# Kernel tuning notes

Hardware: AMD Instinct MI355X
Metric: run time of the kernel (lower is better)

Reference implementation:

```python
import jax, jax.numpy as jnp
import numpy as np
import math

B, C, HW = 4, 256, 32          # batch, seq_len (=channels), spatial side
D_MODEL = HW * HW              # 1024
OUT_C = 32 * 32                # 1024
D_STATE = 16
EXPAND = 2
D_INNER = EXPAND * D_MODEL     # 2048
DT_RANK = math.ceil(D_MODEL / 16)  # 64
D_CONV = 4


def setup_inputs() -> dict:
    key = jax.random.key(0)
    ks = jax.random.split(key, 12)
    s = 0.02
    x1 = jax.random.normal(ks[0], (B, C, HW, HW), dtype=jnp.float32)
    in_proj_w = jax.random.normal(ks[1], (2 * D_INNER, D_MODEL), dtype=jnp.float32) * s
    conv_w = jax.random.normal(ks[2], (D_INNER, 1, D_CONV), dtype=jnp.float32) * s
    conv_b = jnp.zeros((D_INNER,), dtype=jnp.float32)
    x_proj_w = jax.random.normal(ks[3], (DT_RANK + 2 * D_STATE, D_INNER), dtype=jnp.float32) * s
    dt_proj_w = jax.random.normal(ks[4], (D_INNER, DT_RANK), dtype=jnp.float32) * s
    dt_proj_b = jnp.zeros((D_INNER,), dtype=jnp.float32)
    A_log = jnp.log(jnp.broadcast_to(jnp.arange(1, D_STATE + 1, dtype=jnp.float32), (D_INNER, D_STATE)))
    D = jnp.ones((D_INNER,), dtype=jnp.float32)
    out_proj_w = jax.random.normal(ks[5], (OUT_C, D_INNER), dtype=jnp.float32) * s
    ln_w = jnp.ones((OUT_C,), dtype=jnp.float32)
    ln_b = jnp.zeros((OUT_C,), dtype=jnp.float32)
    return {"x1": x1, "in_proj_w": in_proj_w, "conv_w": conv_w, "conv_b": conv_b,
            "x_proj_w": x_proj_w, "dt_proj_w": dt_proj_w, "dt_proj_b": dt_proj_b,
            "A_log": A_log, "D": D, "out_proj_w": out_proj_w, "ln_w": ln_w, "ln_b": ln_b}


def _mamba_forward(x, in_proj_w, conv_w, conv_b, x_proj_w, dt_proj_w, dt_proj_b, A_log, D, out_proj_w):
    # x: (B, L, d_model)
    xz = jnp.einsum('bld,ed->ble', x, in_proj_w)            # (B,L,2*d_inner)
    xs, res = jnp.split(xz, 2, axis=-1)                     # each (B,L,d_inner)
    # depthwise causal conv1d, padding=d_conv-1 then truncate to L (== left pad)
    xs_c = jnp.transpose(xs, (0, 2, 1))                     # (B,d_inner,L)
    xs_c = jax.lax.conv_general_dilated(
        xs_c, conv_w, window_strides=(1,), padding=[(D_CONV - 1, 0)],
        dimension_numbers=('NCH', 'OIH', 'NCH'), feature_group_count=D_INNER)
    xs_c = xs_c + conv_b[None, :, None]
    xs = jax.nn.silu(jnp.transpose(xs_c, (0, 2, 1)))        # (B,L,d_inner)
    # input-dependent SSM parameters
    x_dbl = jnp.einsum('bld,ed->ble', xs, x_proj_w)         # (B,L,dt_rank+2N)
    dt, Bm, Cm = jnp.split(x_dbl, [DT_RANK, DT_RANK + D_STATE], axis=-1)
    delta = jax.nn.softplus(jnp.einsum('blr,dr->bld', dt, dt_proj_w) + dt_proj_b)  # (B,L,d_inner)
    A = -jnp.exp(A_log)                                     # (d_inner, N)
    deltaA = jnp.exp(delta[..., None] * A)                  # (B,L,d_inner,N)
    deltaB_u = delta[..., None] * Bm[:, :, None, :] * xs[..., None]  # (B,L,d_inner,N)

    def step(h, inp):
        dA, dBu, Ct = inp                                   # (B,d,N),(B,d,N),(B,N)
        h = dA * h + dBu
        y = jnp.einsum('bdn,bn->bd', h, Ct)
        return h, y

    h0 = jnp.zeros((deltaA.shape[0], D_INNER, D_STATE), dtype=deltaA.dtype)
    _, ys = jax.lax.scan(step, h0, (jnp.transpose(deltaA, (1, 0, 2, 3)),
                                    jnp.transpose(deltaB_u, (1, 0, 2, 3)),
                                    jnp.transpose(Cm, (1, 0, 2))))
    y = jnp.transpose(ys, (1, 0, 2))                        # (B,L,d_inner)
    y = y + D * xs
    y = y * jax.nn.silu(res)
    return jnp.einsum('bld,od->blo', y, out_proj_w)         # (B,L,out_c)


def reference(x1, in_proj_w, conv_w, conv_b, x_proj_w, dt_proj_w, dt_proj_b,
              A_log, D, out_proj_w, ln_w, ln_b):
    b, c, h, w = x1.shape
    x = x1.reshape(b, c, h * w)                             # (B, L=c, d_model)
    y = _mamba_forward(x, in_proj_w, conv_w, conv_b, x_proj_w, dt_proj_w,
                       dt_proj_b, A_log, D, out_proj_w)
    mu = jnp.mean(y, axis=-1, keepdims=True)
    var = jnp.var(y, axis=-1, keepdims=True)
    y = (y - mu) * jax.lax.rsqrt(var + 1e-5) * ln_w + ln_b
    return y.reshape(b, c, 32, 32)
```

## Files before the change

kernel.cpp:

```cpp
#include <hip/hip_runtime.h>
#include <hip/hip_bf16.h>
#include <math.h>

#define BATCH 4
#define SEQL 256
#define DMODEL 1024
#define DINNER 2048
#define DSTATE 16
#define DTRANK 64
#define OUTC 1024
#define NROWS (BATCH * SEQL)
#define NCHUNK 4
#define CH 64

typedef __attribute__((ext_vector_type(8))) short bf16x8;
typedef __attribute__((ext_vector_type(4))) float f32x4;

__global__ __launch_bounds__(256) void gemm_mfma(const __hip_bfloat16* __restrict__ A,
                                                 const __hip_bfloat16* __restrict__ B,
                                                 float* __restrict__ C,
                                                 int M, int N, int K,
                                                 int lda, int ldb) {
    __shared__ __hip_bfloat16 As[2][128 * 32];
    __shared__ __hip_bfloat16 Bs[2][128 * 32];
    const int t  = threadIdx.x;
    const int w  = t >> 6;
    const int ln = t & 63;
    const int wm = w >> 1, wn = w & 1;
    const int q  = ln >> 4, lr = ln & 15;
    const int m0 = blockIdx.y * 128;
    const int n0 = blockIdx.x * 128;
    const int Kpart = K / gridDim.z;
    const int kbase = blockIdx.z * Kpart;

    f32x4 acc[4][4] = {};

    const __hip_bfloat16* Ag = A + (size_t)m0 * lda + kbase;
    const __hip_bfloat16* Bg = B + (size_t)n0 * ldb + kbase;

    auto stage = [&](int k0, int buf) {
        #pragma unroll
        for (int i = 0; i < 2; ++i) {
            const int c = (i * 4 + w) * 64 + ln;
            const int r = c >> 2, col = (c & 3) * 8;
            __builtin_amdgcn_global_load_lds(
                (const __attribute__((address_space(1))) void*)(Ag + (size_t)r * lda + k0 + col),
                (__attribute__((address_space(3))) void*)(As[buf] + (i * 4 + w) * 64 * 8),
                16, 0, 0);
            __builtin_amdgcn_global_load_lds(
                (const __attribute__((address_space(1))) void*)(Bg + (size_t)r * ldb + k0 + col),
                (__attribute__((address_space(3))) void*)(Bs[buf] + (i * 4 + w) * 64 * 8),
                16, 0, 0);
        }
    };

    const int nk = Kpart / 32;
    stage(0, 0);
    __syncthreads();
    for (int kk = 0; kk < nk; ++kk) {
        if (kk + 1 < nk) stage((kk + 1) * 32, (kk + 1) & 1);
        const int buf = kk & 1;
        bf16x8 af[4], bfr[4];
        #pragma unroll
        for (int i = 0; i < 4; ++i)
            af[i] = *(const bf16x8*)(As[buf] + (wm * 64 + i * 16 + lr) * 32 + q * 8);
        #pragma unroll
        for (int j = 0; j < 4; ++j)
            bfr[j] = *(const bf16x8*)(Bs[buf] + (wn * 64 + j * 16 + lr) * 32 + q * 8);
        #pragma unroll
        for (int i = 0; i < 4; ++i)
            #pragma unroll
            for (int j = 0; j < 4; ++j)
                acc[i][j] = __builtin_amdgcn_mfma_f32_16x16x32_bf16(af[i], bfr[j], acc[i][j], 0, 0, 0);
        __syncthreads();
    }
    float* Cz = C + (size_t)blockIdx.z * M * N;
    #pragma unroll
    for (int i = 0; i < 4; ++i) {
        const int mrow = m0 + wm * 64 + i * 16 + q * 4;
        #pragma unroll
        for (int j = 0; j < 4; ++j) {
            const int ncol = n0 + wn * 64 + j * 16 + lr;
            #pragma unroll
            for (int r = 0; r < 4; ++r)
                Cz[(size_t)(mrow + r) * N + ncol] = acc[i][j][r];
        }
    }
}

__global__ __launch_bounds__(256) void gemm_dtsp(const __hip_bfloat16* __restrict__ A,
                                                 const __hip_bfloat16* __restrict__ B,
                                                 const float* __restrict__ bd,
                                                 float* __restrict__ delta) {
    __shared__ __hip_bfloat16 As[128 * 32];
    __shared__ __hip_bfloat16 Bs[128 * 32];
    const int t  = threadIdx.x;
    const int w  = t >> 6;
    const int ln = t & 63;
    const int wm = w >> 1, wn = w & 1;
    const int q  = ln >> 4, lr = ln & 15;
    const int m0 = blockIdx.y * 128;
    const int n0 = blockIdx.x * 128;
    const int lda = 128, ldb = 64, N = 2048;

    f32x4 acc[4][4] = {};
    const __hip_bfloat16* Ag = A + (size_t)m0 * lda;
    const __hip_bfloat16* Bg = B + (size_t)n0 * ldb;

    for (int k0 = 0; k0 < 64; k0 += 32) {
        #pragma unroll
        for (int i = 0; i < 2; ++i) {
            const int c = (i * 4 + w) * 64 + ln;
            const int r = c >> 2, col = (c & 3) * 8;
            __builtin_amdgcn_global_load_lds(
                (const __attribute__((address_space(1))) void*)(Ag + (size_t)r * lda + k0 + col),
                (__attribute__((address_space(3))) void*)(As + (i * 4 + w) * 64 * 8),
                16, 0, 0);
            __builtin_amdgcn_global_load_lds(
                (const __attribute__((address_space(1))) void*)(Bg + (size_t)r * ldb + k0 + col),
                (__attribute__((address_space(3))) void*)(Bs + (i * 4 + w) * 64 * 8),
                16, 0, 0);
        }
        __syncthreads();
        bf16x8 af[4], bfr[4];
        #pragma unroll
        for (int i = 0; i < 4; ++i)
            af[i] = *(const bf16x8*)(As + (wm * 64 + i * 16 + lr) * 32 + q * 8);
        #pragma unroll
        for (int j = 0; j < 4; ++j)
            bfr[j] = *(const bf16x8*)(Bs + (wn * 64 + j * 16 + lr) * 32 + q * 8);
        #pragma unroll
        for (int i = 0; i < 4; ++i)
            #pragma unroll
            for (int j = 0; j < 4; ++j)
                acc[i][j] = __builtin_amdgcn_mfma_f32_16x16x32_bf16(af[i], bfr[j], acc[i][j], 0, 0, 0);
        __syncthreads();
    }
    #pragma unroll
    for (int i = 0; i < 4; ++i) {
        const int mrow = m0 + wm * 64 + i * 16 + q * 4;
        #pragma unroll
        for (int j = 0; j < 4; ++j) {
            const int ncol = n0 + wn * 64 + j * 16 + lr;
            const float bias = bd[ncol];
            #pragma unroll
            for (int r = 0; r < 4; ++r) {
                float v = acc[i][j][r] + bias;
                float sp = (v > 20.f) ? v : log1pf(__expf(v));
                delta[(size_t)(mrow + r) * N + ncol] = sp;
            }
        }
    }
}

__global__ void xdbl_reduce_kernel(const float* __restrict__ part,
                                   float* __restrict__ xdbl,
                                   __hip_bfloat16* __restrict__ xdblb) {
    const int i = blockIdx.x * 256 + threadIdx.x;
    float s = 0.f;
    #pragma unroll
    for (int z = 0; z < 8; ++z) s += part[(size_t)z * (1024 * 128) + i];
    xdbl[i] = s;
    xdblb[i] = __float2bfloat16(s);
}

#define R0 (1024 * 1024)
#define R1 (R0 + 4096 * 1024)
#define R2 (R1 + 2048 * 1024)
#define R3 (R2 + 128 * 2048)
#define R4 (R3 + 2048 * 64)
__global__ void cast_all_kernel(const float* __restrict__ x1,
                                const float* __restrict__ w_in,
                                const float* __restrict__ w_out,
                                const float* __restrict__ w_xp,
                                const float* __restrict__ w_dt,
                                __hip_bfloat16* __restrict__ xa,
                                __hip_bfloat16* __restrict__ wb1,
                                __hip_bfloat16* __restrict__ wob,
                                __hip_bfloat16* __restrict__ wpb,
                                __hip_bfloat16* __restrict__ wdb) {
    int i = blockIdx.x * 256 + threadIdx.x;
    if (i < R0) {
        xa[i] = __float2bfloat16(x1[i]);
    } else if (i < R1) {
        int j = i - R0; wb1[j] = __float2bfloat16(w_in[j]);
    } else if (i < R2) {
        int j = i - R1; wob[j] = __float2bfloat16(w_out[j]);
    } else if (i < R3) {
        int j = i - R2; int e = j >> 11;
        wpb[j] = __float2bfloat16(e < 96 ? w_xp[j] : 0.f);
    } else if (i < R4) {
        int j = i - R3; wdb[j] = __float2bfloat16(w_dt[j]);
    }
}

__global__ void conv_silu_kernel(const float* __restrict__ xz,
                                 const float* __restrict__ conv_w,
                                 const float* __restrict__ conv_b,
                                 float* __restrict__ xs,
                                 __hip_bfloat16* __restrict__ xsb) {
    int idx = blockIdx.x * blockDim.x + threadIdx.x;
    int d = idx & (DINNER - 1);
    int l = (idx >> 11) & (SEQL - 1);
    int b = idx >> 19;
    const float w0 = conv_w[d * 4 + 0];
    const float w1 = conv_w[d * 4 + 1];
    const float w2 = conv_w[d * 4 + 2];
    const float w3 = conv_w[d * 4 + 3];
    float acc = conv_b[d];
    const size_t base = (size_t)(b * SEQL) * (2 * DINNER) + d;
    if (l >= 3) acc += w0 * xz[base + (size_t)(l - 3) * (2 * DINNER)];
    if (l >= 2) acc += w1 * xz[base + (size_t)(l - 2) * (2 * DINNER)];
    if (l >= 1) acc += w2 * xz[base + (size_t)(l - 1) * (2 * DINNER)];
    acc += w3 * xz[base + (size_t)l * (2 * DINNER)];
    float v = acc / (1.f + __expf(-acc));
    xs[idx] = v;
    xsb[idx] = __float2bfloat16(v);
}

__device__ __forceinline__ float row_reduce16(float x) {
    x += __int_as_float(__builtin_amdgcn_update_dpp(0, __float_as_int(x), 0x128, 0xF, 0xF, true));
    x += __int_as_float(__builtin_amdgcn_update_dpp(0, __float_as_int(x), 0x124, 0xF, 0xF, true));
    x += __int_as_float(__builtin_amdgcn_update_dpp(0, __float_as_int(x), 0x122, 0xF, 0xF, true));
    x += __int_as_float(__builtin_amdgcn_update_dpp(0, __float_as_int(x), 0x121, 0xF, 0xF, true));
    return x;
}

__global__ __launch_bounds__(256) void scan_carry_kernel(const float* __restrict__ delta,
                                                         const float* __restrict__ xs,
                                                         const float* __restrict__ xdbl,
                                                         const float* __restrict__ A_log,
                                                         float* __restrict__ carryL,
                                                         float* __restrict__ carryP) {
    __shared__ float sDU[CH][16][2];
    __shared__ float sB[CH][16];
    const int b = blockIdx.y, c = blockIdx.z, dg = blockIdx.x;
    const int t = threadIdx.x;
    const int dl = t >> 4, n = t & 15;
    const int d = dg * 16 + dl;
    const float a = -__expf(A_log[d * DSTATE + n]);
    const int srow = t >> 4, scol = t & 15;
    const int sd = dg * 16 + scol;
    const int rowbase = b * SEQL + c * CH;
    #pragma unroll
    for (int i = 0; i < 4; ++i) {
        const int row = rowbase + i * 16 + srow;
        const float dv = delta[(size_t)row * DINNER + sd];
        const float xv = xs[(size_t)row * DINNER + sd];
        sDU[i * 16 + srow][scol][0] = dv;
        sDU[i * 16 + srow][scol][1] = dv * xv;
        sB[i * 16 + srow][scol] = xdbl[row * 128 + 64 + scol];
    }
    __syncthreads();
    float h = 0.f, P = 1.f;
    #pragma unroll 16
    for (int l = 0; l < CH; ++l) {
        const float e = __expf(sDU[l][dl][0] * a);
        h = e * h + sDU[l][dl][1] * sB[l][n];
        P *= e;
    }
    const size_t ci = (((size_t)(b * NCHUNK + c)) * DINNER + d) * DSTATE + n;
    carryL[ci] = h;
    carryP[ci] = P;
}

__global__ __launch_bounds__(256) void scan_apply_kernel(const float* __restrict__ delta,
                                                         const float* __restrict__ xs,
                                                         const float* __restrict__ xdbl,
                                                         const float* __restrict__ xz,
                                                         const float* __restrict__ A_log,
                                                         const float* __restrict__ Dp,
                                                         const float* __restrict__ carryL,
                                                         const float* __restrict__ carryP,
                                                         __hip_bfloat16* __restrict__ ybb) {
    __shared__ float sDU[CH][16][2];
    __shared__ float sBC[CH][16][2];
    __shared__ float sGW[CH][16][2];
    const int b = blockIdx.y, c = blockIdx.z, dg = blockIdx.x;
    const int t = threadIdx.x;
    const int dl = t >> 4, n = t & 15;
    const int d = dg * 16 + dl;
    const float a = -__expf(A_log[d * DSTATE + n]);
    const int srow = t >> 4, scol = t & 15;
    const int sd = dg * 16 + scol;
    const float Dstage = Dp[sd];
    const int rowbase = b * SEQL + c * CH;
    #pragma unroll
    for (int i = 0; i < 4; ++i) {
        const int row = rowbase + i * 16 + srow;
        const float dv = delta[(size_t)row * DINNER + sd];
        const float xv = xs[(size_t)row * DINNER + sd];
        const float r  = xz[(size_t)row * (2 * DINNER) + DINNER + sd];
        const float g = r / (1.f + __expf(-r));
        const int lr_ = i * 16 + srow;
        sDU[lr_][scol][0] = dv;
        sDU[lr_][scol][1] = dv * xv;
        sGW[lr_][scol][0] = g;
        sGW[lr_][scol][1] = Dstage * xv * g;
        sBC[lr_][scol][0] = xdbl[row * 128 + 64 + scol];
        sBC[lr_][scol][1] = xdbl[row * 128 + 80 + scol];
    }
    __syncthreads();
    float h = 0.f;
    for (int j = 0; j < c; ++j) {
        const size_t ci = (((size_t)(b * NCHUNK + j)) * DINNER + d) * DSTATE + n;
        h = carryP[ci] * h + carryL[ci];
    }
    #pragma unroll 16
    for (int l = 0; l < CH; ++l) {
        const float e = __expf(sDU[l][dl][0] * a);
        h = e * h + sDU[l][dl][1] * sBC[l][n][0];
        float p = row_reduce16(h * sBC[l][n][1]);
        if (n == 0) {
            const float y = p * sGW[l][dl][0] + sGW[l][dl][1];
            ybb[(size_t)(rowbase + l) * DINNER + d] = __float2bfloat16(y);
        }
    }
}

__global__ __launch_bounds__(256) void ln_kernel(const float* __restrict__ opart,
                                                 const float* __restrict__ lw,
                                                 const float* __restrict__ lb,
                                                 float* __restrict__ out) {
    __shared__ float red[8];
    const int row = blockIdx.x;
    const int t = threadIdx.x;
    float v[4];
    float s = 0.f, s2 = 0.f;
    #pragma unroll
    for (int i = 0; i < 4; ++i) {
        const int c = t + 256 * i;
        float acc = 0.f;
        #pragma unroll
        for (int z = 0; z < 4; ++z)
            acc += opart[(size_t)z * (1024 * 1024) + (size_t)row * OUTC + c];
        v[i] = acc;
        s += acc;
        s2 += acc * acc;
    }
    #pragma unroll
    for (int o = 32; o; o >>= 1) {
        s += __shfl_down(s, o);
        s2 += __shfl_down(s2, o);
    }
    const int wid = t >> 6;
    if ((t & 63) == 0) { red[wid] = s; red[4 + wid] = s2; }
    __syncthreads();
    if (t == 0) {
        float ts = red[0] + red[1] + red[2] + red[3];
        float ts2 = red[4] + red[5] + red[6] + red[7];
        float mu = ts * (1.f / OUTC);
        float var = ts2 * (1.f / OUTC) - mu * mu;
        red[0] = mu;
        red[1] = rsqrtf(var + 1e-5f);
    }
    __syncthreads();
    const float mu = red[0], rs = red[1];
    #pragma unroll
    for (int i = 0; i < 4; ++i) {
        const int c = t + 256 * i;
        out[(size_t)row * OUTC + c] = (v[i] - mu) * rs * lw[c] + lb[c];
    }
}

extern "C" void kernel_launch(void* const* d_in, const int* in_sizes, int n_in,
                              void* d_out, int out_size, void* d_ws, size_t ws_size,
                              hipStream_t stream) {
    const float* x1        = (const float*)d_in[0];
    const float* in_proj_w = (const float*)d_in[1];
    const float* conv_w    = (const float*)d_in[2];
    const float* conv_b    = (const float*)d_in[3];
    const float* x_proj_w  = (const float*)d_in[4];
    const float* dt_proj_w = (const float*)d_in[5];
    const float* dt_proj_b = (const float*)d_in[6];
    const float* A_log     = (const float*)d_in[7];
    const float* Dp        = (const float*)d_in[8];
    const float* out_proj_w= (const float*)d_in[9];
    const float* ln_w      = (const float*)d_in[10];
    const float* ln_b      = (const float*)d_in[11];
    float* out = (float*)d_out;

    char* p = (char*)d_ws;
    __hip_bfloat16* xa    = (__hip_bfloat16*)p; p += (size_t)1024 * 1024 * 2;
    __hip_bfloat16* wb1   = (__hip_bfloat16*)p; p += (size_t)4096 * 1024 * 2;
    __hip_bfloat16* wpb   = (__hip_bfloat16*)p; p += (size_t)128 * 2048 * 2;
    __hip_bfloat16* wob   = (__hip_bfloat16*)p; p += (size_t)1024 * 2048 * 2;
    __hip_bfloat16* wdb   = (__hip_bfloat16*)p; p += (size_t)2048 * 64 * 2;
    __hip_bfloat16* xsb   = (__hip_bfloat16*)p; p += (size_t)1024 * 2048 * 2;
    __hip_bfloat16* ybb   = (__hip_bfloat16*)p; p += (size_t)1024 * 2048 * 2;
    __hip_bfloat16* xdblb = (__hip_bfloat16*)p; p += (size_t)1024 * 128 * 2;
    float* xz    = (float*)p; p += (size_t)1024 * 4096 * 4;
    float* xs    = (float*)p; p += (size_t)1024 * 2048 * 4;
    float* xdbl  = (float*)p; p += (size_t)1024 * 128 * 4;
    float* xpart = (float*)p; p += (size_t)8 * 1024 * 128 * 4;
    float* delta = (float*)p; p += (size_t)1024 * 2048 * 4;
    float* carryL = (float*)p; p += (size_t)BATCH * NCHUNK * DINNER * DSTATE * 4;
    float* carryP = (float*)p; p += (size_t)BATCH * NCHUNK * DINNER * DSTATE * 4;
    float* opart = xz;

    cast_all_kernel<<<(R4 + 255) / 256, 256, 0, stream>>>(x1, in_proj_w, out_proj_w,
                                                          x_proj_w, dt_proj_w,
                                                          xa, wb1, wob, wpb, wdb);
    gemm_mfma<<<dim3(32, 8, 1), 256, 0, stream>>>(xa, wb1, xz,
                                                  NROWS, 2 * DINNER, DMODEL, DMODEL, DMODEL);
    conv_silu_kernel<<<(NROWS * DINNER) / 256, 256, 0, stream>>>(xz, conv_w, conv_b, xs, xsb);
    gemm_mfma<<<dim3(1, 8, 8), 256, 0, stream>>>(xsb, wpb, xpart,
                                                 NROWS, 128, DINNER, DINNER, DINNER);
    xdbl_reduce_kernel<<<(1024 * 128) / 256, 256, 0, stream>>>(xpart, xdbl, xdblb);
    gemm_dtsp<<<dim3(16, 8), 256, 0, stream>>>(xdblb, wdb, dt_proj_b, delta);
    scan_carry_kernel<<<dim3(DINNER / 16, BATCH, NCHUNK), 256, 0, stream>>>(
        delta, xs, xdbl, A_log, carryL, carryP);
    scan_apply_kernel<<<dim3(DINNER / 16, BATCH, NCHUNK), 256, 0, stream>>>(
        delta, xs, xdbl, xz, A_log, Dp, carryL, carryP, ybb);
    gemm_mfma<<<dim3(8, 8, 4), 256, 0, stream>>>(ybb, wob, opart,
                                                 NROWS, OUTC, DINNER, DINNER, DINNER);
    ln_kernel<<<NROWS, 256, 0, stream>>>(opart, ln_w, ln_b, out);
}
```

Measured before the change: 221.1 us.

## Fuse fp32-to-bf16 casts into GEMMs and drop xdbl reduce kernel

```diff
diff --git a/kernel.cpp b/kernel.cpp
--- a/kernel.cpp
+++ b/kernel.cpp
@@ -16,13 +16,94 @@
 typedef __attribute__((ext_vector_type(8))) short bf16x8;
 typedef __attribute__((ext_vector_type(4))) float f32x4;
 
+__device__ __forceinline__ short f2b(float x) {
+    union { __hip_bfloat16 h; short s; } u;
+    u.h = __float2bfloat16(x);
+    return u.s;
+}
+__device__ __forceinline__ float b2f(short x) {
+    union { __hip_bfloat16 h; short s; } u;
+    u.s = x;
+    return __bfloat162float(u.h);
+}
+__device__ __forceinline__ bf16x8 cvt8(const float* p) {
+    bf16x8 r;
+    #pragma unroll
+    for (int j = 0; j < 8; ++j) r[j] = f2b(p[j]);
+    return r;
+}
+
+__global__ __launch_bounds__(256) void gemm_in(const float* __restrict__ A,
+                                               const float* __restrict__ B,
+                                               __hip_bfloat16* __restrict__ C) {
+    const int K = 1024, N = 4096;
+    __shared__ float As[2][128 * 32];
+    __shared__ float Bs[2][128 * 32];
+    const int t  = threadIdx.x;
+    const int w  = t >> 6;
+    const int ln = t & 63;
+    const int wm = w >> 1, wn = w & 1;
+    const int q  = ln >> 4, lr = ln & 15;
+    const int m0 = blockIdx.y * 128;
+    const int n0 = blockIdx.x * 128;
+
+    f32x4 acc[4][4] = {};
+    const float* Ag = A + (size_t)m0 * K;
+    const float* Bg = B + (size_t)n0 * K;
+
+    auto stage = [&](int k0, int buf) {
+        #pragma unroll
+        for (int i = 0; i < 4; ++i) {
+            const int c = (i * 4 + w) * 64 + ln;
+            const int r = c >> 3, col = (c & 7) * 4;
+            __builtin_amdgcn_global_load_lds(
+                (const __attribute__((address_space(1))) void*)(Ag + (size_t)r * K + k0 + col),
+                (__attribute__((address_space(3))) void*)(As[buf] + c * 4), 16, 0, 0);
+            __builtin_amdgcn_global_load_lds(
+                (const __attribute__((address_space(1))) void*)(Bg + (size_t)r * K + k0 + col),
+                (__attribute__((address_space(3))) void*)(Bs[buf] + c * 4), 16, 0, 0);
+        }
+    };
+
+    stage(0, 0);
+    __syncthreads();
+    for (int kk = 0; kk < 32; ++kk) {
+        if (kk + 1 < 32) stage((kk + 1) * 32, (kk + 1) & 1);
+        const int buf = kk & 1;
+        bf16x8 af[4], bfr[4];
+        #pragma unroll
+        for (int i = 0; i < 4; ++i)
+            af[i] = cvt8(As[buf] + (wm * 64 + i * 16 + lr) * 32 + q * 8);
+        #pragma unroll
+        for (int j = 0; j < 4; ++j)
+            bfr[j] = cvt8(Bs[buf] + (wn * 64 + j * 16 + lr) * 32 + q * 8);
+        #pragma unroll
+        for (int i = 0; i < 4; ++i)
+            #pragma unroll
+            for (int j = 0; j < 4; ++j)
+                acc[i][j] = __builtin_amdgcn_mfma_f32_16x16x32_bf16(af[i], bfr[j], acc[i][j], 0, 0, 0);
+        __syncthreads();
+    }
+    #pragma unroll
+    for (int i = 0; i < 4; ++i) {
+        const int mrow = m0 + wm * 64 + i * 16 + q * 4;
+        #pragma unroll
+        for (int j = 0; j < 4; ++j) {
+            const int ncol = n0 + wn * 64 + j * 16 + lr;
+            #pragma unroll
+            for (int r = 0; r < 4; ++r)
+                C[(size_t)(mrow + r) * N + ncol] = __float2bfloat16(acc[i][j][r]);
+        }
+    }
+}
+
 __global__ __launch_bounds__(256) void gemm_mfma(const __hip_bfloat16* __restrict__ A,
                                                  const __hip_bfloat16* __restrict__ B,
                                                  float* __restrict__ C,
                                                  int M, int N, int K,
                                                  int lda, int ldb) {
-    __shared__ __hip_bfloat16 As[2][128 * 32];
-    __shared__ __hip_bfloat16 Bs[2][128 * 32];
+    __shared__ __hip_bfloat16 As[128 * 32];
+    __shared__ __hip_bfloat16 Bs[128 * 32];
     const int t  = threadIdx.x;
     const int w  = t >> 6;
     const int ln = t & 63;
@@ -34,39 +115,29 @@
     const int kbase = blockIdx.z * Kpart;
 
     f32x4 acc[4][4] = {};
-
     const __hip_bfloat16* Ag = A + (size_t)m0 * lda + kbase;
     const __hip_bfloat16* Bg = B + (size_t)n0 * ldb + kbase;
 
-    auto stage = [&](int k0, int buf) {
+    for (int k0 = 0; k0 < Kpart; k0 += 32) {
         #pragma unroll
         for (int i = 0; i < 2; ++i) {
             const int c = (i * 4 + w) * 64 + ln;
             const int r = c >> 2, col = (c & 3) * 8;
             __builtin_amdgcn_global_load_lds(
                 (const __attribute__((address_space(1))) void*)(Ag + (size_t)r * lda + k0 + col),
-                (__attribute__((address_space(3))) void*)(As[buf] + (i * 4 + w) * 64 * 8),
-                16, 0, 0);
+                (__attribute__((address_space(3))) void*)(As + c * 8), 16, 0, 0);
             __builtin_amdgcn_global_load_lds(
                 (const __attribute__((address_space(1))) void*)(Bg + (size_t)r * ldb + k0 + col),
-                (__attribute__((address_space(3))) void*)(Bs[buf] + (i * 4 + w) * 64 * 8),
-                16, 0, 0);
-        }
-    };
-
-    const int nk = Kpart / 32;
-    stage(0, 0);
-    __syncthreads();
-    for (int kk = 0; kk < nk; ++kk) {
-        if (kk + 1 < nk) stage((kk + 1) * 32, (kk + 1) & 1);
-        const int buf = kk & 1;
+                (__attribute__((address_space(3))) void*)(Bs + c * 8), 16, 0, 0);
+        }
+        __syncthreads();
         bf16x8 af[4], bfr[4];
         #pragma unroll
         for (int i = 0; i < 4; ++i)
-            af[i] = *(const bf16x8*)(As[buf] + (wm * 64 + i * 16 + lr) * 32 + q * 8);
+            af[i] = *(const bf16x8*)(As + (wm * 64 + i * 16 + lr) * 32 + q * 8);
         #pragma unroll
         for (int j = 0; j < 4; ++j)
-            bfr[j] = *(const bf16x8*)(Bs[buf] + (wn * 64 + j * 16 + lr) * 32 + q * 8);
+            bfr[j] = *(const bf16x8*)(Bs + (wn * 64 + j * 16 + lr) * 32 + q * 8);
         #pragma unroll
         for (int i = 0; i < 4; ++i)
             #pragma unroll
@@ -88,11 +159,77 @@
     }
 }
 
-__global__ __launch_bounds__(256) void gemm_dtsp(const __hip_bfloat16* __restrict__ A,
-                                                 const __hip_bfloat16* __restrict__ B,
+__global__ __launch_bounds__(256) void gemm_out(const __hip_bfloat16* __restrict__ A,
+                                                const float* __restrict__ B,
+                                                float* __restrict__ C) {
+    const int M = 1024, N = 1024, K = 2048;
+    __shared__ __hip_bfloat16 As[128 * 32];
+    __shared__ float Bs[128 * 32];
+    const int t  = threadIdx.x;
+    const int w  = t >> 6;
+    const int ln = t & 63;
+    const int wm = w >> 1, wn = w & 1;
+    const int q  = ln >> 4, lr = ln & 15;
+    const int m0 = blockIdx.y * 128;
+    const int n0 = blockIdx.x * 128;
+    const int Kpart = K / 4;
+    const int kbase = blockIdx.z * Kpart;
+
+    f32x4 acc[4][4] = {};
+    const __hip_bfloat16* Ag = A + (size_t)m0 * K + kbase;
+    const float* Bg = B + (size_t)n0 * K + kbase;
+
+    for (int k0 = 0; k0 < Kpart; k0 += 32) {
+        #pragma unroll
+        for (int i = 0; i < 2; ++i) {
+            const int c = (i * 4 + w) * 64 + ln;
+            const int r = c >> 2, col = (c & 3) * 8;
+            __builtin_amdgcn_global_load_lds(
+                (const __attribute__((address_space(1))) void*)(Ag + (size_t)r * K + k0 + col),
+                (__attribute__((address_space(3))) void*)(As + c * 8), 16, 0, 0);
+        }
+        #pragma unroll
+        for (int i = 0; i < 4; ++i) {
+            const int c = (i * 4 + w) * 64 + ln;
+            const int r = c >> 3, col = (c & 7) * 4;
+            __builtin_amdgcn_global_load_lds(
+                (const __attribute__((address_space(1))) void*)(Bg + (size_t)r * K + k0 + col),
+                (__attribute__((address_space(3))) void*)(Bs + c * 4), 16, 0, 0);
+        }
+        __syncthreads();
+        bf16x8 af[4], bfr[4];
+        #pragma unroll
+        for (int i = 0; i < 4; ++i)
+            af[i] = *(const bf16x8*)(As + (wm * 64 + i * 16 + lr) * 32 + q * 8);
+        #pragma unroll
+        for (int j = 0; j < 4; ++j)
+            bfr[j] = cvt8(Bs + (wn * 64 + j * 16 + lr) * 32 + q * 8);
+        #pragma unroll
+        for (int i = 0; i < 4; ++i)
+            #pragma unroll
+            for (int j = 0; j < 4; ++j)
+                acc[i][j] = __builtin_amdgcn_mfma_f32_16x16x32_bf16(af[i], bfr[j], acc[i][j], 0, 0, 0);
+        __syncthreads();
+    }
+    float* Cz = C + (size_t)blockIdx.z * M * N;
+    #pragma unroll
+    for (int i = 0; i < 4; ++i) {
+        const int mrow = m0 + wm * 64 + i * 16 + q * 4;
+        #pragma unroll
+        for (int j = 0; j < 4; ++j) {
+            const int ncol = n0 + wn * 64 + j * 16 + lr;
+            #pragma unroll
+            for (int r = 0; r < 4; ++r)
+                Cz[(size_t)(mrow + r) * N + ncol] = acc[i][j][r];
+        }
+    }
+}
+
+__global__ __launch_bounds__(256) void gemm_dtsp(const float* __restrict__ xpart,
+                                                 const __hip_bfloat16* __restrict__ Bw,
                                                  const float* __restrict__ bd,
                                                  float* __restrict__ delta) {
-    __shared__ __hip_bfloat16 As[128 * 32];
+    __shared__ __hip_bfloat16 As[128 * 64];
     __shared__ __hip_bfloat16 Bs[128 * 32];
     const int t  = threadIdx.x;
     const int w  = t >> 6;
@@ -101,31 +238,35 @@
     const int q  = ln >> 4, lr = ln & 15;
     const int m0 = blockIdx.y * 128;
     const int n0 = blockIdx.x * 128;
-    const int lda = 128, ldb = 64, N = 2048;
+    const int N = 2048;
+
+    #pragma unroll
+    for (int j = 0; j < 32; ++j) {
+        const int e = j * 256 + t;
+        const int row = e >> 6, col = e & 63;
+        float s = 0.f;
+        #pragma unroll
+        for (int z = 0; z < 8; ++z)
+            s += xpart[(size_t)z * (1024 * 128) + (size_t)(m0 + row) * 128 + col];
+        As[row * 64 + col] = __float2bfloat16(s);
+    }
 
     f32x4 acc[4][4] = {};
-    const __hip_bfloat16* Ag = A + (size_t)m0 * lda;
-    const __hip_bfloat16* Bg = B + (size_t)n0 * ldb;
-
+    const __hip_bfloat16* Bg = Bw + (size_t)n0 * 64;
     for (int k0 = 0; k0 < 64; k0 += 32) {
         #pragma unroll
         for (int i = 0; i < 2; ++i) {
             const int c = (i * 4 + w) * 64 + ln;
             const int r = c >> 2, col = (c & 3) * 8;
             __builtin_amdgcn_global_load_lds(
-                (const __attribute__((address_space(1))) void*)(Ag + (size_t)r * lda + k0 + col),
-                (__attribute__((address_space(3))) void*)(As + (i * 4 + w) * 64 * 8),
-                16, 0, 0);
-            __builtin_amdgcn_global_load_lds(
-                (const __attribute__((address_space(1))) void*)(Bg + (size_t)r * ldb + k0 + col),
-                (__attribute__((address_space(3))) void*)(Bs + (i * 4 + w) * 64 * 8),
-                16, 0, 0);
+                (const __attribute__((address_space(1))) void*)(Bg + (size_t)r * 64 + k0 + col),
+                (__attribute__((address_space(3))) void*)(Bs + c * 8), 16, 0, 0);
         }
         __syncthreads();
         bf16x8 af[4], bfr[4];
         #pragma unroll
         for (int i = 0; i < 4; ++i)
-            af[i] = *(const bf16x8*)(As + (wm * 64 + i * 16 + lr) * 32 + q * 8);
+            af[i] = *(const bf16x8*)(As + (wm * 64 + i * 16 + lr) * 64 + k0 + q * 8);
         #pragma unroll
         for (int j = 0; j < 4; ++j)
             bfr[j] = *(const bf16x8*)(Bs + (wn * 64 + j * 16 + lr) * 32 + q * 8);
@@ -146,76 +287,48 @@
             #pragma unroll
             for (int r = 0; r < 4; ++r) {
                 float v = acc[i][j][r] + bias;
-                float sp = (v > 20.f) ? v : log1pf(__expf(v));
-                delta[(size_t)(mrow + r) * N + ncol] = sp;
+                delta[(size_t)(mrow + r) * N + ncol] = (v > 20.f) ? v : log1pf(__expf(v));
             }
         }
     }
 }
 
-__global__ void xdbl_reduce_kernel(const float* __restrict__ part,
-                                   float* __restrict__ xdbl,
-                                   __hip_bfloat16* __restrict__ xdblb) {
-    const int i = blockIdx.x * 256 + threadIdx.x;
-    float s = 0.f;
-    #pragma unroll
-    for (int z = 0; z < 8; ++z) s += part[(size_t)z * (1024 * 128) + i];
-    xdbl[i] = s;
-    xdblb[i] = __float2bfloat16(s);
-}
-
-#define R0 (1024 * 1024)
-#define R1 (R0 + 4096 * 1024)
-#define R2 (R1 + 2048 * 1024)
-#define R3 (R2 + 128 * 2048)
-#define R4 (R3 + 2048 * 64)
-__global__ void cast_all_kernel(const float* __restrict__ x1,
-                                const float* __restrict__ w_in,
-                                const float* __restrict__ w_out,
-                                const float* __restrict__ w_xp,
-                                const float* __restrict__ w_dt,
-                                __hip_bfloat16* __restrict__ xa,
-                                __hip_bfloat16* __restrict__ wb1,
-                                __hip_bfloat16* __restrict__ wob,
-                                __hip_bfloat16* __restrict__ wpb,
-                                __hip_bfloat16* __restrict__ wdb) {
-    int i = blockIdx.x * 256 + threadIdx.x;
-    if (i < R0) {
-        xa[i] = __float2bfloat16(x1[i]);
-    } else if (i < R1) {
-        int j = i - R0; wb1[j] = __float2bfloat16(w_in[j]);
-    } else if (i < R2) {
-        int j = i - R1; wob[j] = __float2bfloat16(w_out[j]);
-    } else if (i < R3) {
-        int j = i - R2; int e = j >> 11;
-        wpb[j] = __float2bfloat16(e < 96 ? w_xp[j] : 0.f);
-    } else if (i < R4) {
-        int j = i - R3; wdb[j] = __float2bfloat16(w_dt[j]);
-    }
-}
-
-__global__ void conv_silu_kernel(const float* __restrict__ xz,
+__global__ void conv_silu_kernel(const __hip_bfloat16* __restrict__ xz,
                                  const float* __restrict__ conv_w,
                                  const float* __restrict__ conv_b,
+                                 const float* __restrict__ w_xp,
+                                 const float* __restrict__ w_dt,
                                  float* __restrict__ xs,
-                                 __hip_bfloat16* __restrict__ xsb) {
-    int idx = blockIdx.x * blockDim.x + threadIdx.x;
-    int d = idx & (DINNER - 1);
-    int l = (idx >> 11) & (SEQL - 1);
-    int b = idx >> 19;
-    const float w0 = conv_w[d * 4 + 0];
-    const float w1 = conv_w[d * 4 + 1];
-    const float w2 = conv_w[d * 4 + 2];
-    const float w3 = conv_w[d * 4 + 3];
-    float acc = conv_b[d];
-    const size_t base = (size_t)(b * SEQL) * (2 * DINNER) + d;
-    if (l >= 3) acc += w0 * xz[base + (size_t)(l - 3) * (2 * DINNER)];
-    if (l >= 2) acc += w1 * xz[base + (size_t)(l - 2) * (2 * DINNER)];
-    if (l >= 1) acc += w2 * xz[base + (size_t)(l - 1) * (2 * DINNER)];
-    acc += w3 * xz[base + (size_t)l * (2 * DINNER)];
-    float v = acc / (1.f + __expf(-acc));
-    xs[idx] = v;
-    xsb[idx] = __float2bfloat16(v);
+                                 __hip_bfloat16* __restrict__ xsb,
+                                 __hip_bfloat16* __restrict__ wpb,
+                                 __hip_bfloat16* __restrict__ wdb) {
+    const int bid = blockIdx.x;
+    if (bid < 8192) {
+        int idx = bid * 256 + threadIdx.x;
+        int d = idx & (DINNER - 1);
+        int l = (idx >> 11) & (SEQL - 1);
+        int b = idx >> 19;
+        const float w0 = conv_w[d * 4 + 0];
+        const float w1 = conv_w[d * 4 + 1];
+        const float w2 = conv_w[d * 4 + 2];
+        const float w3 = conv_w[d * 4 + 3];
+        float acc = conv_b[d];
+        const size_t base = (size_t)(b * SEQL) * 4096 + d;
+        if (l >= 3) acc += w0 * __bfloat162float(xz[base + (size_t)(l - 3) * 4096]);
+        if (l >= 2) acc += w1 * __bfloat162float(xz[base + (size_t)(l - 2) * 4096]);
+        if (l >= 1) acc += w2 * __bfloat162float(xz[base + (size_t)(l - 1) * 4096]);
+        acc += w3 * __bfloat162float(xz[base + (size_t)l * 4096]);
+        float v = acc / (1.f + __expf(-acc));
+        xs[idx] = v;
+        xsb[idx] = __float2bfloat16(v);
+    } else if (bid < 8192 + 1024) {
+        int j = (bid - 8192) * 256 + threadIdx.x;
+        int e = j >> 11;
+        wpb[j] = __float2bfloat16(e < 96 ? w_xp[j] : 0.f);
+    } else {
+        int j = (bid - 9216) * 256 + threadIdx.x;
+        wdb[j] = __float2bfloat16(w_dt[j]);
+    }
 }
 
 __device__ __forceinline__ float row_reduce16(float x) {
@@ -226,12 +339,12 @@
     return x;
 }
 
-__global__ __launch_bounds__(256) void scan_carry_kernel(const float* __restrict__ delta,
-                                                         const float* __restrict__ xs,
-                                                         const float* __restrict__ xdbl,
-                                                         const float* __restrict__ A_log,
-                                                         float* __restrict__ carryL,
-                                                         float* __restrict__ carryP) {
+__global__ __launch_bounds__(256, 8) void scan_carry_kernel(const float* __restrict__ delta,
+                                                            const float* __restrict__ xs,
+                                                            const float* __restrict__ xpart,
+                                                            const float* __restrict__ A_log,
+                                                            float* __restrict__ carryL,
+                                                            float* __restrict__ carryP) {
     __shared__ float sDU[CH][16][2];
     __shared__ float sB[CH][16];
     const int b = blockIdx.y, c = blockIdx.z, dg = blockIdx.x;
@@ -249,7 +362,11 @@
         const float xv = xs[(size_t)row * DINNER + sd];
         sDU[i * 16 + srow][scol][0] = dv;
         sDU[i * 16 + srow][scol][1] = dv * xv;
-        sB[i * 16 + srow][scol] = xdbl[row * 128 + 64 + scol];
+        float bsum = 0.f;
+        #pragma unroll
+        for (int z = 0; z < 8; ++z)
+            bsum += xpart[(size_t)z * (1024 * 128) + (size_t)row * 128 + 64 + scol];
+        sB[i * 16 + srow][scol] = bsum;
     }
     __syncthreads();
     float h = 0.f, P = 1.f;
@@ -264,18 +381,19 @@
     carryP[ci] = P;
 }
 
-__global__ __launch_bounds__(256) void scan_apply_kernel(const float* __restrict__ delta,
-                                                         const float* __restrict__ xs,
-                                                         const float* __restrict__ xdbl,
-                                                         const float* __restrict__ xz,
-                                                         const float* __restrict__ A_log,
-                                                         const float* __restrict__ Dp,
-                                                         const float* __restrict__ carryL,
-                                                         const float* __restrict__ carryP,
-                                                         __hip_bfloat16* __restrict__ ybb) {
+__global__ __launch_bounds__(256, 8) void scan_apply_kernel(const float* __restrict__ delta,
+                                                            const float* __restrict__ xs,
+                                                            const float* __restrict__ xpart,
+                                                            const __hip_bfloat16* __restrict__ xz,
+                                                            const float* __restrict__ A_log,
+                                                            const float* __restrict__ Dp,
+                                                            const float* __restrict__ carryL,
+                                                            const float* __restrict__ carryP,
+                                                            __hip_bfloat16* __restrict__ ybb) {
     __shared__ float sDU[CH][16][2];
     __shared__ float sBC[CH][16][2];
-    __shared__ float sGW[CH][16][2];
+    __shared__ short sRES[CH][16];
+    __shared__ short sXW[CH][16];
     const int b = blockIdx.y, c = blockIdx.z, dg = blockIdx.x;
     const int t = threadIdx.x;
     const int dl = t >> 4, n = t & 15;
@@ -288,17 +406,22 @@
     #pragma unroll
     for (int i = 0; i < 4; ++i) {
         const int row = rowbase + i * 16 + srow;
+        const int lr_ = i * 16 + srow;
         const float dv = delta[(size_t)row * DINNER + sd];
         const float xv = xs[(size_t)row * DINNER + sd];
-        const float r  = xz[(size_t)row * (2 * DINNER) + DINNER + sd];
-        const float g = r / (1.f + __expf(-r));
-        const int lr_ = i * 16 + srow;
         sDU[lr_][scol][0] = dv;
         sDU[lr_][scol][1] = dv * xv;
-        sGW[lr_][scol][0] = g;
-        sGW[lr_][scol][1] = Dstage * xv * g;
-        sBC[lr_][scol][0] = xdbl[row * 128 + 64 + scol];
-        sBC[lr_][scol][1] = xdbl[row * 128 + 80 + scol];
+        sXW[lr_][scol] = f2b(Dstage * xv);
+        sRES[lr_][scol] = ((const short*)xz)[(size_t)row * 4096 + DINNER + sd];
+        float bsum = 0.f, csum = 0.f;
+        #pragma unroll
+        for (int z = 0; z < 8; ++z) {
+            const size_t pb = (size_t)z * (1024 * 128) + (size_t)row * 128;
+            bsum += xpart[pb + 64 + scol];
+            csum += xpart[pb + 80 + scol];
+        }
+        sBC[lr_][scol][0] = bsum;
+        sBC[lr_][scol][1] = csum;
     }
     __syncthreads();
     float h = 0.f;
@@ -312,7 +435,9 @@
         h = e * h + sDU[l][dl][1] * sBC[l][n][0];
         float p = row_reduce16(h * sBC[l][n][1]);
         if (n == 0) {
-            const float y = p * sGW[l][dl][0] + sGW[l][dl][1];
+            const float r = b2f(sRES[l][dl]);
+            const float g = r / (1.f + __expf(-r));
+            const float y = g * (p + b2f(sXW[l][dl]));
             ybb[(size_t)(rowbase + l) * DINNER + d] = __float2bfloat16(y);
         }
     }
@@ -381,38 +506,28 @@
     float* out = (float*)d_out;
 
     char* p = (char*)d_ws;
-    __hip_bfloat16* xa    = (__hip_bfloat16*)p; p += (size_t)1024 * 1024 * 2;
-    __hip_bfloat16* wb1   = (__hip_bfloat16*)p; p += (size_t)4096 * 1024 * 2;
-    __hip_bfloat16* wpb   = (__hip_bfloat16*)p; p += (size_t)128 * 2048 * 2;
-    __hip_bfloat16* wob   = (__hip_bfloat16*)p; p += (size_t)1024 * 2048 * 2;
-    __hip_bfloat16* wdb   = (__hip_bfloat16*)p; p += (size_t)2048 * 64 * 2;
-    __hip_bfloat16* xsb   = (__hip_bfloat16*)p; p += (size_t)1024 * 2048 * 2;
-    __hip_bfloat16* ybb   = (__hip_bfloat16*)p; p += (size_t)1024 * 2048 * 2;
-    __hip_bfloat16* xdblb = (__hip_bfloat16*)p; p += (size_t)1024 * 128 * 2;
-    float* xz    = (float*)p; p += (size_t)1024 * 4096 * 4;
-    float* xs    = (float*)p; p += (size_t)1024 * 2048 * 4;
-    float* xdbl  = (float*)p; p += (size_t)1024 * 128 * 4;
-    float* xpart = (float*)p; p += (size_t)8 * 1024 * 128 * 4;
-    float* delta = (float*)p; p += (size_t)1024 * 2048 * 4;
+    __hip_bfloat16* xz   = (__hip_bfloat16*)p; p += (size_t)1024 * 4096 * 2;
+    __hip_bfloat16* xsb  = (__hip_bfloat16*)p; p += (size_t)1024 * 2048 * 2;
+    __hip_bfloat16* ybb  = (__hip_bfloat16*)p; p += (size_t)1024 * 2048 * 2;
+    __hip_bfloat16* wpb  = (__hip_bfloat16*)p; p += (size_t)128 * 2048 * 2;
+    __hip_bfloat16* wdb  = (__hip_bfloat16*)p; p += (size_t)2048 * 64 * 2;
+    float* xs     = (float*)p; p += (size_t)1024 * 2048 * 4;
+    float* xpart  = (float*)p; p += (size_t)8 * 1024 * 128 * 4;
+    float* delta  = (float*)p; p += (size_t)1024 * 2048 * 4;
     float* carryL = (float*)p; p += (size_t)BATCH * NCHUNK * DINNER * DSTATE * 4;
     float* carryP = (float*)p; p += (size_t)BATCH * NCHUNK * DINNER * DSTATE * 4;
-    float* opart = xz;
-
-    cast_all_kernel<<<(R4 + 255) / 256, 256, 0, stream>>>(x1, in_proj_w, out_proj_w,
-                                                          x_proj_w, dt_proj_w,
-                                                          xa, wb1, wob, wpb, wdb);
-    gemm_mfma<<<dim3(32, 8, 1), 256, 0, stream>>>(xa, wb1, xz,
-                                                  NROWS, 2 * DINNER, DMODEL, DMODEL, DMODEL);
-    conv_silu_kernel<<<(NROWS * DINNER) / 256, 256, 0, stream>>>(xz, conv_w, conv_b, xs, xsb);
+    float* opart  = (float*)p; p += (size_t)4 * 1024 * 1024 * 4;
+
+    gemm_in<<<dim3(32, 8), 256, 0, stream>>>(x1, in_proj_w, xz);
+    conv_silu_kernel<<<9728, 256, 0, stream>>>(xz, conv_w, conv_b, x_proj_w, dt_proj_w,
+                                               xs, xsb, wpb, wdb);
     gemm_mfma<<<dim3(1, 8, 8), 256, 0, stream>>>(xsb, wpb, xpart,
                                                  NROWS, 128, DINNER, DINNER, DINNER);
-    xdbl_reduce_kernel<<<(1024 * 128) / 256, 256, 0, stream>>>(xpart, xdbl, xdblb);
-    gemm_dtsp<<<dim3(16, 8), 256, 0, stream>>>(xdblb, wdb, dt_proj_b, delta);
-    scan_carry_kernel<<<dim3(DINNER / 16, BATCH, NCHUNK), 256, 0, stream>>>(
-        delta, xs, xdbl, A_log, carryL, carryP);
-    scan_apply_kernel<<<dim3(DINNER / 16, BATCH, NCHUNK), 256, 0, stream>>>(
-        delta, xs, xdbl, xz, A_log, Dp, carryL, carryP, ybb);
-    gemm_mfma<<<dim3(8, 8, 4), 256, 0, stream>>>(ybb, wob, opart,
-                                                 NROWS, OUTC, DINNER, DINNER, DINNER);
+    gemm_dtsp<<<dim3(16, 8), 256, 0, stream>>>(xpart, wdb, dt_proj_b, delta);
+    scan_carry_kernel<<<dim3(128, BATCH, NCHUNK), 256, 0, stream>>>(
+        delta, xs, xpart, A_log, carryL, carryP);
+    scan_apply_kernel<<<dim3(128, BATCH, NCHUNK), 256, 0, stream>>>(
+        delta, xs, xpart, xz, A_log, Dp, carryL, carryP, ybb);
+    gemm_out<<<dim3(8, 8, 4), 256, 0, stream>>>(ybb, out_proj_w, opart);
     ln_kernel<<<NROWS, 256, 0, stream>>>(opart, ln_w, ln_b, out);
 }
```

After: 369.3 us. +67.0%, slower.
